# Performance work log

Hardware: AMD Instinct MI355X
Metric: run time of the kernel (lower is better)

Reference implementation:

```python
import jax, jax.numpy as jnp
import numpy as np
from jax import lax

WINDOW_SIZE = 11
SIGMA = 1.5
DATA_RANGE = 1.0
EPS = 1e-8


def _gauss_1d(window_size=WINDOW_SIZE, sigma=SIGMA):
    coords = jnp.arange(window_size, dtype=jnp.float32) - window_size // 2
    g = jnp.exp(-(coords ** 2) / (2.0 * sigma ** 2))
    return g / g.sum()


def _gaussian_filter(x, w1d):
    # Separable depthwise blur: horizontal then vertical, VALID padding (use_padding=False).
    C = x.shape[1]
    win = w1d.shape[0]
    kh = jnp.broadcast_to(w1d.reshape(1, 1, 1, win), (C, 1, 1, win))  # OIHW, groups=C
    kv = jnp.broadcast_to(w1d.reshape(1, 1, win, 1), (C, 1, win, 1))
    dn = ('NCHW', 'OIHW', 'NCHW')
    out = lax.conv_general_dilated(x, kh, (1, 1), 'VALID',
                                   dimension_numbers=dn, feature_group_count=C)
    out = lax.conv_general_dilated(out, kv, (1, 1), 'VALID',
                                   dimension_numbers=dn, feature_group_count=C)
    return out


def setup_inputs() -> dict:
    key = jax.random.key(0)
    k1, k2 = jax.random.split(key)
    B, C, H, W = 16, 3, 768, 768
    X = jax.random.uniform(k1, (B, C, H, W), dtype=jnp.float32)
    Y = jax.random.uniform(k2, (B, C, H, W), dtype=jnp.float32)
    window = _gauss_1d()
    return {"X": X, "Y": Y, "window": window}


def reference(X, Y, window):
    K1, K2 = 0.01, 0.03
    C1 = (K1 * DATA_RANGE) ** 2
    C2 = (K2 * DATA_RANGE) ** 2
    mu_x = _gaussian_filter(X, window)
    mu_y = _gaussian_filter(Y, window)
    sigma_x = _gaussian_filter(X * X, window) - mu_x ** 2
    sigma_y = _gaussian_filter(Y * Y, window) - mu_y ** 2
    sigma_xy = _gaussian_filter(X * Y, window) - mu_x * mu_y
    cs = (2.0 * sigma_xy + C2) / (sigma_x + sigma_y + C2 + EPS)
    cs = jax.nn.relu(cs)
    ssim_map = (2.0 * mu_x * mu_y + C1) / (mu_x ** 2 + mu_y ** 2 + C1 + EPS) * cs
    ssim_val = ssim_map.mean(axis=(1, 2, 3))  # [B]
    return ssim_val
```

## Files before the change

### kernel.cpp

```cpp
#include <hip/hip_runtime.h>


#define H_IMG 768
#define W_IMG 768
#define OH 758
#define OW_TOT 758
#define OWS 256
#define NSEG 8

__global__ void ssim_zero_out(float* __restrict__ out) {
    if (threadIdx.x < 16) out[threadIdx.x] = 0.0f;
}

__launch_bounds__(256, 3)
__global__ void ssim_fused(const float* __restrict__ X, const float* __restrict__ Y,
                           const float* __restrict__ Wg, float* __restrict__ out) {
    const float C1 = 1e-4f, C2 = 9e-4f, EPS = 1e-8f;
    const float INV_COUNT = 1.0f / (3.0f * 758.0f * 758.0f);

    const int t = threadIdx.x;
    int bx = blockIdx.x;
    const int seg = bx & 7; bx >>= 3;
    const int strip = bx % 3; bx /= 3;
    const int ch = bx % 3;
    const int b  = bx / 3;

    const int R0 = (OH * seg) / NSEG;
    const int R1 = (OH * (seg + 1)) / NSEG;
    const int c0 = strip * OWS;

    const float* Xi = X + (size_t)(b * 3 + ch) * (H_IMG * W_IMG);
    const float* Yi = Y + (size_t)(b * 3 + ch) * (H_IMG * W_IMG);

    float w[11];
#pragma unroll
    for (int k = 0; k < 11; ++k) w[k] = Wg[k];

    __shared__ float hbuf[4][5][OWS];
    __shared__ float red[4];

    const int sA = t >> 6;
    const int cg = t & 63;
    const int colbase = c0 + 4 * cg;
    const int k0 = min(colbase,      W_IMG - 4);
    const int k1 = min(colbase + 4,  W_IMG - 4);
    const int k2 = min(colbase + 8,  W_IMG - 4);
    const int k3 = min(colbase + 12, W_IMG - 2);

    float ring[5][14];
#pragma unroll
    for (int q = 0; q < 5; ++q)
#pragma unroll
        for (int j = 0; j < 14; ++j) ring[q][j] = 0.0f;

    float local = 0.0f;
    const int M = (R1 - R0 + 13) >> 2;

    for (int m = 0; m < M; ++m) {
        {
            int r = R0 + 4 * m + sA;
            r = min(r, H_IMG - 1);
            const float* xr = Xi + (size_t)r * W_IMG;
            const float* yr = Yi + (size_t)r * W_IMG;
            float4 xa = *(const float4*)(xr + k0);
            float4 xb = *(const float4*)(xr + k1);
            float4 xc = *(const float4*)(xr + k2);
            float2 xd = *(const float2*)(xr + k3);
            float4 ya = *(const float4*)(yr + k0);
            float4 yb = *(const float4*)(yr + k1);
            float4 yc = *(const float4*)(yr + k2);
            float2 yd = *(const float2*)(yr + k3);
            float xv[14] = {xa.x, xa.y, xa.z, xa.w, xb.x, xb.y, xb.z, xb.w,
                            xc.x, xc.y, xc.z, xc.w, xd.x, xd.y};
            float yv[14] = {ya.x, ya.y, ya.z, ya.w, yb.x, yb.y, yb.z, yb.w,
                            yc.x, yc.y, yc.z, yc.w, yd.x, yd.y};

            float h0[4] = {0,0,0,0}, h1[4] = {0,0,0,0}, h4[4] = {0,0,0,0};
#pragma unroll
            for (int k = 0; k < 11; ++k)
#pragma unroll
                for (int cc = 0; cc < 4; ++cc) {
                    h0[cc] = fmaf(w[k], xv[cc + k], h0[cc]);
                    h1[cc] = fmaf(w[k], yv[cc + k], h1[cc]);
                    h4[cc] = fmaf(w[k], xv[cc + k] * yv[cc + k], h4[cc]);
                }
#pragma unroll
            for (int p = 0; p < 14; ++p) { xv[p] *= xv[p]; yv[p] *= yv[p]; }
            float h2[4] = {0,0,0,0}, h3[4] = {0,0,0,0};
#pragma unroll
            for (int k = 0; k < 11; ++k)
#pragma unroll
                for (int cc = 0; cc < 4; ++cc) {
                    h2[cc] = fmaf(w[k], xv[cc + k], h2[cc]);
                    h3[cc] = fmaf(w[k], yv[cc + k], h3[cc]);
                }
            *(float4*)&hbuf[sA][0][4 * cg] = make_float4(h0[0], h0[1], h0[2], h0[3]);
            *(float4*)&hbuf[sA][1][4 * cg] = make_float4(h1[0], h1[1], h1[2], h1[3]);
            *(float4*)&hbuf[sA][2][4 * cg] = make_float4(h2[0], h2[1], h2[2], h2[3]);
            *(float4*)&hbuf[sA][3][4 * cg] = make_float4(h3[0], h3[1], h3[2], h3[3]);
            *(float4*)&hbuf[sA][4][4 * cg] = make_float4(h4[0], h4[1], h4[2], h4[3]);
        }
        __syncthreads();

        {
#pragma unroll
            for (int q = 0; q < 5; ++q)
#pragma unroll
                for (int j = 0; j < 10; ++j) ring[q][j] = ring[q][j + 4];
#pragma unroll
            for (int s2 = 0; s2 < 4; ++s2)
#pragma unroll
                for (int q = 0; q < 5; ++q)
                    ring[q][10 + s2] = hbuf[s2][q][t];

            const bool colok = (c0 + t) < OW_TOT;
#pragma unroll
            for (int s2 = 0; s2 < 4; ++s2) {
                const int orow = R0 + 4 * m - 10 + s2;
                float a0 = 0.f, a1 = 0.f, a2 = 0.f, a3 = 0.f, a4 = 0.f;
#pragma unroll
                for (int k = 0; k < 11; ++k) {
                    a0 = fmaf(w[k], ring[0][s2 + k], a0);
                    a1 = fmaf(w[k], ring[1][s2 + k], a1);
                    a2 = fmaf(w[k], ring[2][s2 + k], a2);
                    a3 = fmaf(w[k], ring[3][s2 + k], a3);
                    a4 = fmaf(w[k], ring[4][s2 + k], a4);
                }
                float sx  = a2 - a0 * a0;
                float sy  = a3 - a1 * a1;
                float sxy = a4 - a0 * a1;
                float cs = __fdividef(2.0f * sxy + C2, sx + sy + C2 + EPS);
                cs = fmaxf(cs, 0.0f);
                float l = __fdividef(2.0f * a0 * a1 + C1,
                                     a0 * a0 + a1 * a1 + C1 + EPS);
                float v = l * cs;
                if (colok && (orow >= R0) && (orow < R1)) local += v;
            }
        }
        __syncthreads();
    }

    float v = local;
#pragma unroll
    for (int off = 32; off > 0; off >>= 1) v += __shfl_down(v, off, 64);
    if ((t & 63) == 0) red[t >> 6] = v;
    __syncthreads();
    if (t == 0) {
        atomicAdd(&out[b], (red[0] + red[1] + red[2] + red[3]) * INV_COUNT);
    }
}

extern "C" void kernel_launch(void* const* d_in, const int* in_sizes, int n_in,
                              void* d_out, int out_size, void* d_ws, size_t ws_size,
                              hipStream_t stream) {
    const float* X  = (const float*)d_in[0];
    const float* Y  = (const float*)d_in[1];
    const float* Wg = (const float*)d_in[2];
    float* out = (float*)d_out;

    hipLaunchKernelGGL(ssim_zero_out, dim3(1), dim3(64), 0, stream, out);
    hipLaunchKernelGGL(ssim_fused, dim3(16 * 3 * 3 * NSEG), dim3(256), 0, stream,
                       X, Y, Wg, out);
}
```

Baseline: 327.8 us.

## Pack x/y filter channels into float2 FMAs, double row segments, raise occupancy

Interleaves the x and y blur channels (and their squares) as two-wide float vectors so both the horizontal and vertical passes can use packed FMA instructions. The intermediate shared buffers are laid out to match, so one 8-byte LDS read serves two channels. Row segments per image go from 8 to 16, and the launch bound asks for 4 blocks per SIMD. More segments mean more halo rows recomputed per block, and the tighter register budget may cause spills.

Result: slower. 354.0 us (+8.0%).

```diff
diff --git a/kernel.cpp b/kernel.cpp
--- a/kernel.cpp
+++ b/kernel.cpp
@@ -1,18 +1,28 @@
 #include <hip/hip_runtime.h>
 
+
+typedef float f32x2 __attribute__((ext_vector_type(2)));
+typedef float f32x4 __attribute__((ext_vector_type(4)));
 
 #define H_IMG 768
 #define W_IMG 768
 #define OH 758
 #define OW_TOT 758
 #define OWS 256
-#define NSEG 8
+#define NSEG 16
+
+static __device__ __forceinline__ f32x2 mk2(float a, float b) {
+    f32x2 r; r.x = a; r.y = b; return r;
+}
+static __device__ __forceinline__ f32x4 mk4(float a, float b, float c, float d) {
+    f32x4 r; r.x = a; r.y = b; r.z = c; r.w = d; return r;
+}
 
 __global__ void ssim_zero_out(float* __restrict__ out) {
     if (threadIdx.x < 16) out[threadIdx.x] = 0.0f;
 }
 
-__launch_bounds__(256, 3)
+__launch_bounds__(256, 4)
 __global__ void ssim_fused(const float* __restrict__ X, const float* __restrict__ Y,
                            const float* __restrict__ Wg, float* __restrict__ out) {
     const float C1 = 1e-4f, C2 = 9e-4f, EPS = 1e-8f;
@@ -20,7 +30,7 @@
 
     const int t = threadIdx.x;
     int bx = blockIdx.x;
-    const int seg = bx & 7; bx >>= 3;
+    const int seg = bx & (NSEG - 1); bx >>= 4;
     const int strip = bx % 3; bx /= 3;
     const int ch = bx % 3;
     const int b  = bx / 3;
@@ -36,7 +46,9 @@
 #pragma unroll
     for (int k = 0; k < 11; ++k) w[k] = Wg[k];
 
-    __shared__ float hbuf[4][5][OWS];
+    __shared__ __align__(16) f32x2 hxyL[4][OWS];
+    __shared__ __align__(16) f32x2 hsqL[4][OWS];
+    __shared__ __align__(16) float hpL[4][OWS];
     __shared__ float red[4];
 
     const int sA = t >> 6;
@@ -47,11 +59,10 @@
     const int k2 = min(colbase + 8,  W_IMG - 4);
     const int k3 = min(colbase + 12, W_IMG - 2);
 
-    float ring[5][14];
+    f32x2 r01[14], r23[14];
+    float r4[14];
 #pragma unroll
-    for (int q = 0; q < 5; ++q)
-#pragma unroll
-        for (int j = 0; j < 14; ++j) ring[q][j] = 0.0f;
+    for (int j = 0; j < 14; ++j) { r01[j] = mk2(0.f, 0.f); r23[j] = mk2(0.f, 0.f); r4[j] = 0.f; }
 
     float local = 0.0f;
     const int M = (R1 - R0 + 13) >> 2;
@@ -75,57 +86,66 @@
             float yv[14] = {ya.x, ya.y, ya.z, ya.w, yb.x, yb.y, yb.z, yb.w,
                             yc.x, yc.y, yc.z, yc.w, yd.x, yd.y};
 
-            float h0[4] = {0,0,0,0}, h1[4] = {0,0,0,0}, h4[4] = {0,0,0,0};
+            f32x2 vxy[14], vsq[14];
+            float vp[14];
 #pragma unroll
-            for (int k = 0; k < 11; ++k)
+            for (int j = 0; j < 14; ++j) {
+                vxy[j] = mk2(xv[j], yv[j]);
+                vp[j]  = xv[j] * yv[j];
+                vsq[j] = vxy[j] * vxy[j];
+            }
+
+            f32x2 hxyA[4], hsqA[4];
+            float hpA[4];
 #pragma unroll
-                for (int cc = 0; cc < 4; ++cc) {
-                    h0[cc] = fmaf(w[k], xv[cc + k], h0[cc]);
-                    h1[cc] = fmaf(w[k], yv[cc + k], h1[cc]);
-                    h4[cc] = fmaf(w[k], xv[cc + k] * yv[cc + k], h4[cc]);
+            for (int cc = 0; cc < 4; ++cc) {
+                f32x2 hxy = mk2(0.f, 0.f), hsq = mk2(0.f, 0.f);
+                float hp = 0.f;
+#pragma unroll
+                for (int k = 0; k < 11; ++k) {
+                    f32x2 ww = mk2(w[k], w[k]);
+                    hxy = __builtin_elementwise_fma(ww, vxy[cc + k], hxy);
+                    hsq = __builtin_elementwise_fma(ww, vsq[cc + k], hsq);
+                    hp  = fmaf(w[k], vp[cc + k], hp);
                 }
-#pragma unroll
-            for (int p = 0; p < 14; ++p) { xv[p] *= xv[p]; yv[p] *= yv[p]; }
-            float h2[4] = {0,0,0,0}, h3[4] = {0,0,0,0};
-#pragma unroll
-            for (int k = 0; k < 11; ++k)
-#pragma unroll
-                for (int cc = 0; cc < 4; ++cc) {
-                    h2[cc] = fmaf(w[k], xv[cc + k], h2[cc]);
-                    h3[cc] = fmaf(w[k], yv[cc + k], h3[cc]);
-                }
-            *(float4*)&hbuf[sA][0][4 * cg] = make_float4(h0[0], h0[1], h0[2], h0[3]);
-            *(float4*)&hbuf[sA][1][4 * cg] = make_float4(h1[0], h1[1], h1[2], h1[3]);
-            *(float4*)&hbuf[sA][2][4 * cg] = make_float4(h2[0], h2[1], h2[2], h2[3]);
-            *(float4*)&hbuf[sA][3][4 * cg] = make_float4(h3[0], h3[1], h3[2], h3[3]);
-            *(float4*)&hbuf[sA][4][4 * cg] = make_float4(h4[0], h4[1], h4[2], h4[3]);
+                hxyA[cc] = hxy; hsqA[cc] = hsq; hpA[cc] = hp;
+            }
+            *(f32x4*)&hxyL[sA][4 * cg]     = mk4(hxyA[0].x, hxyA[0].y, hxyA[1].x, hxyA[1].y);
+            *(f32x4*)&hxyL[sA][4 * cg + 2] = mk4(hxyA[2].x, hxyA[2].y, hxyA[3].x, hxyA[3].y);
+            *(f32x4*)&hsqL[sA][4 * cg]     = mk4(hsqA[0].x, hsqA[0].y, hsqA[1].x, hsqA[1].y);
+            *(f32x4*)&hsqL[sA][4 * cg + 2] = mk4(hsqA[2].x, hsqA[2].y, hsqA[3].x, hsqA[3].y);
+            *(f32x4*)&hpL[sA][4 * cg]      = mk4(hpA[0], hpA[1], hpA[2], hpA[3]);
         }
         __syncthreads();
 
         {
 #pragma unroll
-            for (int q = 0; q < 5; ++q)
+            for (int j = 0; j < 10; ++j) {
+                r01[j] = r01[j + 4];
+                r23[j] = r23[j + 4];
+                r4[j]  = r4[j + 4];
+            }
 #pragma unroll
-                for (int j = 0; j < 10; ++j) ring[q][j] = ring[q][j + 4];
-#pragma unroll
-            for (int s2 = 0; s2 < 4; ++s2)
-#pragma unroll
-                for (int q = 0; q < 5; ++q)
-                    ring[q][10 + s2] = hbuf[s2][q][t];
+            for (int s2 = 0; s2 < 4; ++s2) {
+                r01[10 + s2] = hxyL[s2][t];
+                r23[10 + s2] = hsqL[s2][t];
+                r4[10 + s2]  = hpL[s2][t];
+            }
 
             const bool colok = (c0 + t) < OW_TOT;
 #pragma unroll
             for (int s2 = 0; s2 < 4; ++s2) {
                 const int orow = R0 + 4 * m - 10 + s2;
-                float a0 = 0.f, a1 = 0.f, a2 = 0.f, a3 = 0.f, a4 = 0.f;
+                f32x2 a01 = mk2(0.f, 0.f), a23 = mk2(0.f, 0.f);
+                float a4 = 0.f;
 #pragma unroll
                 for (int k = 0; k < 11; ++k) {
-                    a0 = fmaf(w[k], ring[0][s2 + k], a0);
-                    a1 = fmaf(w[k], ring[1][s2 + k], a1);
-                    a2 = fmaf(w[k], ring[2][s2 + k], a2);
-                    a3 = fmaf(w[k], ring[3][s2 + k], a3);
-                    a4 = fmaf(w[k], ring[4][s2 + k], a4);
+                    f32x2 ww = mk2(w[k], w[k]);
+                    a01 = __builtin_elementwise_fma(ww, r01[s2 + k], a01);
+                    a23 = __builtin_elementwise_fma(ww, r23[s2 + k], a23);
+                    a4  = fmaf(w[k], r4[s2 + k], a4);
                 }
+                float a0 = a01.x, a1 = a01.y, a2 = a23.x, a3 = a23.y;
                 float sx  = a2 - a0 * a0;
                 float sy  = a3 - a1 * a1;
                 float sxy = a4 - a0 * a1;
```

## Merge x²+y² into one blurred field and use a rotating register ring

Applied to the files above, without the earlier changes.

The kernel now blurs x²+y² as a single field, since only sigma_x+sigma_y is needed. This cuts the blurred fields from five to four, which reduces horizontal and vertical FMAs and LDS traffic. The main loop is unrolled by four with a modulo-indexed register ring, which removes the per-iteration register shifting. The two SSIM divisions are combined into one and the row segments double to 16 for more blocks. Applying the ReLU to the full product instead of only the cs term matches the reference only when the luminance term is positive, as it is for non-negative images.

After: 325.8 us. Within noise of the previous version (-0.6%).

```diff
diff --git a/kernel.cpp b/kernel.cpp
--- a/kernel.cpp
+++ b/kernel.cpp
@@ -6,13 +6,13 @@
 #define OH 758
 #define OW_TOT 758
 #define OWS 256
-#define NSEG 8
+#define NSEG 16
 
 __global__ void ssim_zero_out(float* __restrict__ out) {
     if (threadIdx.x < 16) out[threadIdx.x] = 0.0f;
 }
 
-__launch_bounds__(256, 3)
+__attribute__((amdgpu_flat_work_group_size(256, 256), amdgpu_waves_per_eu(3, 3)))
 __global__ void ssim_fused(const float* __restrict__ X, const float* __restrict__ Y,
                            const float* __restrict__ Wg, float* __restrict__ out) {
     const float C1 = 1e-4f, C2 = 9e-4f, EPS = 1e-8f;
@@ -20,13 +20,14 @@
 
     const int t = threadIdx.x;
     int bx = blockIdx.x;
-    const int seg = bx & 7; bx >>= 3;
+    const int seg = bx & (NSEG - 1); bx >>= 4;
     const int strip = bx % 3; bx /= 3;
     const int ch = bx % 3;
     const int b  = bx / 3;
 
     const int R0 = (OH * seg) / NSEG;
-    const int R1 = (OH * (seg + 1)) / NSEG;
+    const int Rend = (OH * (seg + 1)) / NSEG;
+    const int hseg = Rend - R0;
     const int c0 = strip * OWS;
 
     const float* Xi = X + (size_t)(b * 3 + ch) * (H_IMG * W_IMG);
@@ -36,7 +37,7 @@
 #pragma unroll
     for (int k = 0; k < 11; ++k) w[k] = Wg[k];
 
-    __shared__ float hbuf[4][5][OWS];
+    __shared__ float hb[4][4][OWS];
     __shared__ float red[4];
 
     const int sA = t >> 6;
@@ -47,97 +48,97 @@
     const int k2 = min(colbase + 8,  W_IMG - 4);
     const int k3 = min(colbase + 12, W_IMG - 2);
 
-    float ring[5][14];
+    float rg[4][16];
 #pragma unroll
-    for (int q = 0; q < 5; ++q)
+    for (int f = 0; f < 4; ++f)
 #pragma unroll
-        for (int j = 0; j < 14; ++j) ring[q][j] = 0.0f;
+        for (int j = 0; j < 16; ++j) rg[f][j] = 0.0f;
 
+    const bool colok = (c0 + t) < OW_TOT;
     float local = 0.0f;
-    const int M = (R1 - R0 + 13) >> 2;
+    const int M = (hseg + 13) >> 2;
 
-    for (int m = 0; m < M; ++m) {
-        {
-            int r = R0 + 4 * m + sA;
-            r = min(r, H_IMG - 1);
-            const float* xr = Xi + (size_t)r * W_IMG;
-            const float* yr = Yi + (size_t)r * W_IMG;
-            float4 xa = *(const float4*)(xr + k0);
-            float4 xb = *(const float4*)(xr + k1);
-            float4 xc = *(const float4*)(xr + k2);
-            float2 xd = *(const float2*)(xr + k3);
-            float4 ya = *(const float4*)(yr + k0);
-            float4 yb = *(const float4*)(yr + k1);
-            float4 yc = *(const float4*)(yr + k2);
-            float2 yd = *(const float2*)(yr + k3);
-            float xv[14] = {xa.x, xa.y, xa.z, xa.w, xb.x, xb.y, xb.z, xb.w,
-                            xc.x, xc.y, xc.z, xc.w, xd.x, xd.y};
-            float yv[14] = {ya.x, ya.y, ya.z, ya.w, yb.x, yb.y, yb.z, yb.w,
-                            yc.x, yc.y, yc.z, yc.w, yd.x, yd.y};
+    for (int mb = 0; mb < M; mb += 4) {
+#pragma unroll
+        for (int p = 0; p < 4; ++p) {
+            const int m = mb + p;
+            if (m < M) {
+                {
+                    int r = R0 + 4 * m + sA;
+                    r = min(r, H_IMG - 1);
+                    const float* xr = Xi + (size_t)r * W_IMG;
+                    const float* yr = Yi + (size_t)r * W_IMG;
+                    float4 xa = *(const float4*)(xr + k0);
+                    float4 xb = *(const float4*)(xr + k1);
+                    float4 xc = *(const float4*)(xr + k2);
+                    float2 xd = *(const float2*)(xr + k3);
+                    float4 ya = *(const float4*)(yr + k0);
+                    float4 yb = *(const float4*)(yr + k1);
+                    float4 yc = *(const float4*)(yr + k2);
+                    float2 yd = *(const float2*)(yr + k3);
+                    float xv[14] = {xa.x, xa.y, xa.z, xa.w, xb.x, xb.y, xb.z, xb.w,
+                                    xc.x, xc.y, xc.z, xc.w, xd.x, xd.y};
+                    float yv[14] = {ya.x, ya.y, ya.z, ya.w, yb.x, yb.y, yb.z, yb.w,
+                                    yc.x, yc.y, yc.z, yc.w, yd.x, yd.y};
+                    float sv[14], pv[14];
+#pragma unroll
+                    for (int j = 0; j < 14; ++j) {
+                        pv[j] = xv[j] * yv[j];
+                        sv[j] = fmaf(xv[j], xv[j], yv[j] * yv[j]);
+                    }
+                    float h0[4], h1[4], h2[4], h3[4];
+#pragma unroll
+                    for (int cc = 0; cc < 4; ++cc) {
+                        float a0 = 0.f, a1 = 0.f, a2 = 0.f, a3 = 0.f;
+#pragma unroll
+                        for (int k = 0; k < 11; ++k) {
+                            a0 = fmaf(w[k], xv[cc + k], a0);
+                            a1 = fmaf(w[k], yv[cc + k], a1);
+                            a2 = fmaf(w[k], sv[cc + k], a2);
+                            a3 = fmaf(w[k], pv[cc + k], a3);
+                        }
+                        h0[cc] = a0; h1[cc] = a1; h2[cc] = a2; h3[cc] = a3;
+                    }
+                    *(float4*)&hb[sA][0][4 * cg] = make_float4(h0[0], h0[1], h0[2], h0[3]);
+                    *(float4*)&hb[sA][1][4 * cg] = make_float4(h1[0], h1[1], h1[2], h1[3]);
+                    *(float4*)&hb[sA][2][4 * cg] = make_float4(h2[0], h2[1], h2[2], h2[3]);
+                    *(float4*)&hb[sA][3][4 * cg] = make_float4(h3[0], h3[1], h3[2], h3[3]);
+                }
+                __syncthreads();
 
-            float h0[4] = {0,0,0,0}, h1[4] = {0,0,0,0}, h4[4] = {0,0,0,0};
+                {
 #pragma unroll
-            for (int k = 0; k < 11; ++k)
+                    for (int s2 = 0; s2 < 4; ++s2) {
 #pragma unroll
-                for (int cc = 0; cc < 4; ++cc) {
-                    h0[cc] = fmaf(w[k], xv[cc + k], h0[cc]);
-                    h1[cc] = fmaf(w[k], yv[cc + k], h1[cc]);
-                    h4[cc] = fmaf(w[k], xv[cc + k] * yv[cc + k], h4[cc]);
+                        for (int f = 0; f < 4; ++f)
+                            rg[f][(4 * p + s2) & 15] = hb[s2][f][t];
+                    }
+#pragma unroll
+                    for (int s2 = 0; s2 < 4; ++s2) {
+                        const int orel = 4 * m - 10 + s2;
+                        float a0 = 0.f, a1 = 0.f, a2 = 0.f, a3 = 0.f;
+#pragma unroll
+                        for (int k = 0; k < 11; ++k) {
+                            const int sl = (4 * p + s2 + k + 6) & 15;
+                            a0 = fmaf(w[k], rg[0][sl], a0);
+                            a1 = fmaf(w[k], rg[1][sl], a1);
+                            a2 = fmaf(w[k], rg[2][sl], a2);
+                            a3 = fmaf(w[k], rg[3][sl], a3);
+                        }
+                        const float mux2 = a0 * a0;
+                        const float muy2 = a1 * a1;
+                        const float mxy  = a0 * a1;
+                        const float sigsum = a2 - mux2 - muy2;
+                        const float sxy    = a3 - mxy;
+                        const float num = (2.0f * mxy + C1) * (2.0f * sxy + C2);
+                        const float den = (mux2 + muy2 + C1 + EPS) * (sigsum + C2 + EPS);
+                        const float v = fmaxf(__fdividef(num, den), 0.0f);
+                        if (colok && (orel >= 0) && (orel < hseg)) local += v;
+                    }
                 }
-#pragma unroll
-            for (int p = 0; p < 14; ++p) { xv[p] *= xv[p]; yv[p] *= yv[p]; }
-            float h2[4] = {0,0,0,0}, h3[4] = {0,0,0,0};
-#pragma unroll
-            for (int k = 0; k < 11; ++k)
-#pragma unroll
-                for (int cc = 0; cc < 4; ++cc) {
-                    h2[cc] = fmaf(w[k], xv[cc + k], h2[cc]);
-                    h3[cc] = fmaf(w[k], yv[cc + k], h3[cc]);
-                }
-            *(float4*)&hbuf[sA][0][4 * cg] = make_float4(h0[0], h0[1], h0[2], h0[3]);
-            *(float4*)&hbuf[sA][1][4 * cg] = make_float4(h1[0], h1[1], h1[2], h1[3]);
-            *(float4*)&hbuf[sA][2][4 * cg] = make_float4(h2[0], h2[1], h2[2], h2[3]);
-            *(float4*)&hbuf[sA][3][4 * cg] = make_float4(h3[0], h3[1], h3[2], h3[3]);
-            *(float4*)&hbuf[sA][4][4 * cg] = make_float4(h4[0], h4[1], h4[2], h4[3]);
-        }
-        __syncthreads();
-
-        {
-#pragma unroll
-            for (int q = 0; q < 5; ++q)
-#pragma unroll
-                for (int j = 0; j < 10; ++j) ring[q][j] = ring[q][j + 4];
-#pragma unroll
-            for (int s2 = 0; s2 < 4; ++s2)
-#pragma unroll
-                for (int q = 0; q < 5; ++q)
-                    ring[q][10 + s2] = hbuf[s2][q][t];
-
-            const bool colok = (c0 + t) < OW_TOT;
-#pragma unroll
-            for (int s2 = 0; s2 < 4; ++s2) {
-                const int orow = R0 + 4 * m - 10 + s2;
-                float a0 = 0.f, a1 = 0.f, a2 = 0.f, a3 = 0.f, a4 = 0.f;
-#pragma unroll
-                for (int k = 0; k < 11; ++k) {
-                    a0 = fmaf(w[k], ring[0][s2 + k], a0);
-                    a1 = fmaf(w[k], ring[1][s2 + k], a1);
-                    a2 = fmaf(w[k], ring[2][s2 + k], a2);
-                    a3 = fmaf(w[k], ring[3][s2 + k], a3);
-                    a4 = fmaf(w[k], ring[4][s2 + k], a4);
-                }
-                float sx  = a2 - a0 * a0;
-                float sy  = a3 - a1 * a1;
-                float sxy = a4 - a0 * a1;
-                float cs = __fdividef(2.0f * sxy + C2, sx + sy + C2 + EPS);
-                cs = fmaxf(cs, 0.0f);
-                float l = __fdividef(2.0f * a0 * a1 + C1,
-                                     a0 * a0 + a1 * a1 + C1 + EPS);
-                float v = l * cs;
-                if (colok && (orow >= R0) && (orow < R1)) local += v;
+                __syncthreads();
             }
         }
-        __syncthreads();
     }
 
     float v = local;
```
